# Performance work log

Measured on AMD Instinct MI355X. Metric: run time of the kernel, lower is better.

## Reference

```python
import jax, jax.numpy as jnp
import numpy as np

B, S, D = 1, 2048, 2048
H, HD = 16, 128  # n_heads, head_dim
ROPE_BASE = 100000.0


def setup_inputs() -> dict:
    key = jax.random.key(0)
    k0, k1, k2 = jax.random.split(key, 3)
    x = jax.random.normal(k0, (B, S, D), jnp.float32)
    # real RoPE table: (seq_len, head_dim//2, 2) holding (cos, sin)
    inv_freq = 1.0 / (ROPE_BASE ** (np.arange(0, HD, 2, dtype=np.float64) / HD))
    t = np.arange(S, dtype=np.float64)[:, None] * inv_freq[None, :]
    freqs_cis = jnp.asarray(np.stack([np.cos(t), np.sin(t)], axis=-1), jnp.float32)
    input_pos = jnp.arange(S, dtype=jnp.int32)
    Wqkv = jax.random.normal(k1, (D, 3 * D), jnp.float32) * (D ** -0.5)
    bqkv = jnp.zeros((3 * D,), jnp.float32)
    Wdense = jax.random.normal(k2, (D, D), jnp.float32) * (D ** -0.5)
    bdense = jnp.zeros((D,), jnp.float32)
    return {"x": x, "freqs_cis": freqs_cis, "input_pos": input_pos,
            "Wqkv": Wqkv, "bqkv": bqkv, "Wdense": Wdense, "bdense": bdense}


def apply_rotary_emb(x, freqs_cis):
    # x: [B, S, H, HD]; freqs_cis: [S, HD//2, 2]
    xs = x.reshape(*x.shape[:-1], -1, 2)  # [B,S,H,HD/2,2]
    fc = freqs_cis.reshape(1, xs.shape[1], 1, xs.shape[3], 2)
    out = jnp.stack([
        xs[..., 0] * fc[..., 0] - xs[..., 1] * fc[..., 1],
        xs[..., 1] * fc[..., 0] + xs[..., 0] * fc[..., 1],
    ], axis=-1)
    return out.reshape(x.shape).astype(x.dtype)


def reference(x, freqs_cis, input_pos, Wqkv, bqkv, Wdense, bdense):
    b, s, d = x.shape
    qkv = x @ Wqkv + bqkv                      # fused QKV projection
    q, k, v = jnp.split(qkv, 3, axis=-1)
    q = q.reshape(b, s, H, HD)
    k = k.reshape(b, s, H, HD)
    v = v.reshape(b, s, H, HD)
    q = apply_rotary_emb(q, freqs_cis)
    k = apply_rotary_emb(k, freqs_cis)
    # KV-cache update (cache batch = 1, max_seq = context_length)
    k_cache = jnp.zeros((1, S, H, HD), jnp.float32)
    v_cache = jnp.zeros((1, S, H, HD), jnp.float32)
    k_full = k_cache.at[:, input_pos].set(k)
    v_full = v_cache.at[:, input_pos].set(v)
    # causal SDPA in [B, H, S, HD] layout
    qh = q.transpose(0, 2, 1, 3)
    kh = k_full.transpose(0, 2, 1, 3)
    vh = v_full.transpose(0, 2, 1, 3)
    scale = HD ** -0.5
    scores = jnp.einsum('bhqd,bhkd->bhqk', qh, kh) * scale  # [B,H,S,S]
    causal = jnp.tril(jnp.ones((s, S), dtype=bool))
    scores = jnp.where(causal, scores, jnp.finfo(scores.dtype).min)
    attn = jax.nn.softmax(scores, axis=-1)
    ctx = jnp.einsum('bhqk,bhkd->bhqd', attn, vh)
    ctx = ctx.transpose(0, 2, 1, 3).reshape(b, s, d)
    return ctx @ Wdense + bdense
```

## Files before the change

### kernel.cpp

```cpp
#include <hip/hip_runtime.h>

#define S 2048
#define D 2048
#define H 16
#define HD 128
#define N3 6144

typedef __attribute__((ext_vector_type(8))) _Float16 f16x8;
typedef __attribute__((ext_vector_type(4))) float f32x4;
typedef unsigned short ushort_t;
typedef unsigned int uint_t;

__device__ __forceinline__ ushort_t f16_rne(float f) {
    _Float16 h = (_Float16)f;
    return __builtin_bit_cast(ushort_t, h);
}
__device__ __forceinline__ float f16_f32(ushort_t u) {
    return (float)__builtin_bit_cast(_Float16, u);
}

__global__ __launch_bounds__(256) void convert_f16_kernel(
    const float* __restrict__ in, ushort_t* __restrict__ hi)
{
    const int i = blockIdx.x * 256 + threadIdx.x;
    float4 v = ((const float4*)in)[i];
    ((ushort4*)hi)[i] = make_ushort4(f16_rne(v.x), f16_rne(v.y),
                                     f16_rne(v.z), f16_rne(v.w));
}

__global__ __launch_bounds__(256) void convert_t_kernel(
    const float* __restrict__ in, ushort_t* __restrict__ hi,
    int Kdim, int Ndim)
{
    __shared__ float tile[32][33];
    const int k0 = blockIdx.x * 32, n0 = blockIdx.y * 32;
    const int tx = threadIdx.x & 31, ty = threadIdx.x >> 5;
    #pragma unroll
    for (int r = 0; r < 4; r++)
        tile[ty + r * 8][tx] = in[(size_t)(k0 + ty + r * 8) * Ndim + n0 + tx];
    __syncthreads();
    const int n  = threadIdx.x >> 3;
    const int kc = (threadIdx.x & 7) * 4;
    const float v0 = tile[kc + 0][n], v1 = tile[kc + 1][n];
    const float v2 = tile[kc + 2][n], v3 = tile[kc + 3][n];
    const size_t off = (size_t)(n0 + n) * Kdim + k0 + kc;
    *(ushort4*)&hi[off] = make_ushort4(f16_rne(v0), f16_rne(v1),
                                       f16_rne(v2), f16_rne(v3));
}

__device__ __forceinline__ void gload16(const ushort_t* g, ushort_t* l) {
    __builtin_amdgcn_global_load_lds(
        (const __attribute__((address_space(1))) unsigned int*)g,
        (__attribute__((address_space(3))) unsigned int*)l, 16, 0, 0);
}

__device__ __forceinline__ void vwait8() { asm volatile("s_waitcnt vmcnt(8)" ::: "memory"); }
__device__ __forceinline__ void vwait4() { asm volatile("s_waitcnt vmcnt(4)" ::: "memory"); }
__device__ __forceinline__ void vwait0() { asm volatile("s_waitcnt vmcnt(0)" ::: "memory"); }
__device__ __forceinline__ void lwait0() { asm volatile("s_waitcnt lgkmcnt(0)" ::: "memory"); }

#define QNT 32

__device__ __forceinline__ void mm_core_8ph(
    const ushort_t* __restrict__ At, const ushort_t* __restrict__ Bt,
    ushort_t* lds, const int t, f32x4 (&acc)[4][4])
{
    const int w = t >> 6, lane = t & 63;
    const int lr = lane & 15, quad = lane >> 4;
    const int wm = (w & 1) * 64;
    const int wn = (w >> 1) * 64;

    const int srow = lane >> 2;
    const int scol = (lane & 3) * 8;
    const size_t goff0 = (size_t)(w * 16 + srow) * D + scol;
    const size_t goff1 = goff0 + (size_t)64 * D;
    const int ldst0 = w * 512;
    const int ldst1 = 2048 + w * 512;

    auto stage = [&](int j, int Tt) {
        const ushort_t* gb = (j & 1) ? Bt : At;
        const size_t off = (size_t)Tt * 64 + (j >> 1) * 32;
        ushort_t* dst = lds + (Tt & 1) * 16384 + j * 4096;
        gload16(gb + goff0 + off, dst + ldst0);
        gload16(gb + goff1 + off, dst + ldst1);
    };

    const int aro = (wm + lr) * 32 + quad * 8;
    const int bro = 4096 + (wn + lr) * 32 + quad * 8;

    stage(0, 0); stage(1, 0); stage(2, 0); stage(3, 0);
    stage(0, 1); stage(1, 1);
    vwait4();
    __builtin_amdgcn_sched_barrier(0);
    __builtin_amdgcn_s_barrier();

    f16x8 af[4], bf[4];

#define PH(kk, DOSTAGE, ST, WAITN)                                         \
    {                                                                      \
        const ushort_t* base = lds + (T & 1) * 16384 + (kk) * 8192;        \
        _Pragma("unroll")                                                  \
        for (int i = 0; i < 4; i++)                                        \
            af[i] = *(const f16x8*)&base[aro + i * 512];                   \
        _Pragma("unroll")                                                  \
        for (int n = 0; n < 4; n++)                                        \
            bf[n] = *(const f16x8*)&base[bro + n * 512];                   \
        if (DOSTAGE) {                                                     \
            stage((kk) ? 0 : 2, ST);                                       \
            stage((kk) ? 1 : 3, ST);                                       \
        }                                                                  \
        __builtin_amdgcn_s_barrier();                                      \
        lwait0();                                                          \
        __builtin_amdgcn_sched_barrier(0);                                 \
        __builtin_amdgcn_s_setprio(1);                                     \
        _Pragma("unroll")                                                  \
        for (int i = 0; i < 4; i++)                                        \
            _Pragma("unroll")                                              \
            for (int n = 0; n < 4; n++)                                    \
                acc[i][n] = __builtin_amdgcn_mfma_f32_16x16x32_f16(        \
                    af[i], bf[n], acc[i][n], 0, 0, 0);                     \
        __builtin_amdgcn_s_setprio(0);                                     \
        WAITN;                                                             \
        __builtin_amdgcn_s_barrier();                                      \
    }

    for (int T = 0; T < QNT - 2; T++) {
        PH(0, true, T + 1, vwait8());
        PH(1, true, T + 2, vwait8());
    }
    {
        const int T = QNT - 2;
        PH(0, true,  T + 1, vwait8());
        PH(1, false, 0,     vwait4());
    }
    {
        const int T = QNT - 1;
        PH(0, false, 0, vwait0());
        PH(1, false, 0, );
    }
#undef PH
}

__global__ __launch_bounds__(256, 2) void gemm_qkv_mfma(
    const ushort_t* __restrict__ xh,
    const ushort_t* __restrict__ Wth,
    const float* __restrict__ bias, const float* __restrict__ freqs,
    const int* __restrict__ input_pos,
    ushort_t* __restrict__ qhg, ushort_t* __restrict__ khg,
    ushort_t* __restrict__ vhg)
{
    __shared__ ushort_t lds[32768];
    const int t = threadIdx.x;
    const int col0 = blockIdx.x * 128;
    const int row0 = blockIdx.y * 128;

    f32x4 acc[4][4] = {};
    mm_core_8ph(xh + (size_t)row0 * D, Wth + (size_t)col0 * D, lds, t, acc);

    const int lane = t & 63;
    const int quad = lane >> 4;
    const int lr   = lane & 15;
    const int w = t >> 6;
    const int wm = (w & 1) * 64;
    const int wn = (w >> 1) * 64;

    const int which = col0 >> 11;
    const int hh = (col0 & 2047) >> 7;

    if (which == 2) {
        ushort_t* vh_b = vhg + (size_t)hh * HD * S;
        #pragma unroll
        for (int nt = 0; nt < 4; nt++) {
            const int d = wn + nt * 16 + lr;
            const float bsc = bias[col0 + d];
            #pragma unroll
            for (int mt = 0; mt < 4; mt++) {
                #pragma unroll
                for (int reg = 0; reg < 4; reg++) {
                    const int m = row0 + wm + mt * 16 + quad * 4 + reg;
                    const float v = acc[mt][nt][reg] + bsc;
                    vh_b[(size_t)d * S + input_pos[m]] = f16_rne(v);
                }
            }
        }
    } else {
        ushort_t* oh_b = ((which == 0) ? qhg : khg) + (size_t)hh * S * HD;
        #pragma unroll
        for (int nt = 0; nt < 4; nt++) {
            const int d = wn + nt * 16 + lr;
            const float bsc = bias[col0 + d];
            #pragma unroll
            for (int mt = 0; mt < 4; mt++) {
                #pragma unroll
                for (int reg = 0; reg < 4; reg++) {
                    const int m = row0 + wm + mt * 16 + quad * 4 + reg;
                    const float v = acc[mt][nt][reg] + bsc;
                    const float* fc = &freqs[((size_t)m * 64 + (d >> 1)) * 2];
                    const float cc = fc[0], ss = fc[1];
                    const float p = __shfl_xor(v, 1);
                    const float o = (d & 1) ? (v * cc + p * ss) : (v * cc - p * ss);
                    const ushort_t hv = f16_rne(o);
                    const int hp = __shfl_xor((int)hv, 1);
                    if (!(d & 1)) {
                        const int srowg = (which == 0) ? m : input_pos[m];
                        *(uint_t*)&oh_b[(size_t)srowg * HD + d] =
                            (uint_t)hv | ((uint_t)hp << 16);
                    }
                }
            }
        }
    }
}

__global__ __launch_bounds__(256, 2) void gemm_dense_mfma(
    const ushort_t* __restrict__ Ah,
    const ushort_t* __restrict__ Wth,
    const float* __restrict__ bias, float* __restrict__ out)
{
    __shared__ ushort_t lds[32768];
    const int t = threadIdx.x;
    const int col0 = blockIdx.x * 128;
    const int row0 = blockIdx.y * 128;

    f32x4 acc[4][4] = {};
    mm_core_8ph(Ah + (size_t)row0 * D, Wth + (size_t)col0 * D, lds, t, acc);

    const int lane = t & 63;
    const int quad = lane >> 4;
    const int lr   = lane & 15;
    const int w = t >> 6;
    const int wm = (w & 1) * 64;
    const int wn = (w >> 1) * 64;

    #pragma unroll
    for (int nt = 0; nt < 4; nt++) {
        const int n = col0 + wn + nt * 16 + lr;
        const float bsc = bias[n];
        #pragma unroll
        for (int mt = 0; mt < 4; mt++) {
            #pragma unroll
            for (int reg = 0; reg < 4; reg++) {
                const int m = row0 + wm + mt * 16 + quad * 4 + reg;
                const float o = acc[mt][nt][reg] + bsc;
                const float po = __shfl_xor(o, 1);
                if (!(n & 1))
                    *(float2*)&out[(size_t)m * D + n] = make_float2(o, po);
            }
        }
    }
}

__global__ __launch_bounds__(256, 2) void attn_mfma_kernel(
    const ushort_t* __restrict__ qhg, const ushort_t* __restrict__ khg,
    const ushort_t* __restrict__ vhg,
    float* __restrict__ Opart, float* __restrict__ MLpart)
{
    __shared__ ushort_t Khs[2][4096];
    __shared__ ushort_t Vhs[2][4096];
    __shared__ ushort_t Ps[64 * 32];

    const int bi   = blockIdx.x;
    const int h    = (bi & 7) + 8 * ((bi >> 3) & 1);
    const int half = (bi >> 4) & 1;
    const int qi   = bi >> 5;
    const int r = (h & 8) ? qi : (31 - qi);
    const int q0 = r * 64;
    const int nhalf = r + 1;
    const int kt0 = half * nhalf;
    const int kt1 = kt0 + nhalf;
    const int t = threadIdx.x;
    const int w = t >> 6, lane = t & 63;
    const int lr = lane & 15, quad = lane >> 4;

    const size_t qrow = (size_t)h * S + q0 + w * 16 + lr;
    f16x8 qf[4];
    #pragma unroll
    for (int ks = 0; ks < 4; ks++)
        qf[ks] = *(const f16x8*)&qhg[qrow * HD + ks * 32 + quad * 8];

    const ushort_t* kh_b = khg + (size_t)h * S * HD;
    const ushort_t* vh_b = vhg + (size_t)h * HD * S;

    const int keyq = lane >> 2;
    const int sub  = lane & 3;

    auto stage = [&](int kt, int buf) {
        const int k0 = kt * 32;
        #pragma unroll
        for (int hf = 0; hf < 2; hf++) {
            const size_t ksrc = (size_t)(k0 + hf * 16 + keyq) * HD + w * 32 + sub * 8;
            gload16(kh_b + ksrc, &Khs[buf][w * 1024 + hf * 512]);
            const int dim = w * 32 + hf * 16 + keyq;
            const size_t vsrc = (size_t)dim * S + k0 + sub * 8;
            gload16(vh_b + vsrc, &Vhs[buf][(w * 32 + hf * 16) * 32]);
        }
    };

    f32x4 O[8] = {};
    f32x4 Ol = {0.f, 0.f, 0.f, 0.f};
    float mrow[4];
    #pragma unroll
    for (int rr = 0; rr < 4; rr++) mrow[rr] = -1e30f;

    f16x8 onesv;
    #pragma unroll
    for (int i = 0; i < 8; i++) onesv[i] = (_Float16)1.0f;

    const float kSc = 0.08838834764831845f * 1.4426950408889634f;

    stage(kt0, 0);

    for (int kt = kt0; kt < kt1; kt++) {
        const int k0 = kt * 32;
        const int cur = (kt - kt0) & 1;
        __syncthreads();

        if (kt + 1 < kt1) stage(kt + 1, cur ^ 1);

        f32x4 sa[2];
        #pragma unroll
        for (int nt = 0; nt < 2; nt++) {
            f32x4 s = {0.f, 0.f, 0.f, 0.f};
            #pragma unroll
            for (int ks = 0; ks < 4; ks++) {
                f16x8 kf = *(const f16x8*)&Khs[cur][ks * 1024 + (nt * 16 + lr) * 32 + quad * 8];
                s = __builtin_amdgcn_mfma_f32_16x16x32_f16(qf[ks], kf, s, 0, 0, 0);
            }
            sa[nt] = s;
        }

        const int rowbase = q0 + w * 16 + quad * 4;
        const bool need_mask = (k0 + 31) > (q0 + w * 16);
        float alpha[4], pv0[4], pv1[4];
        #pragma unroll
        for (int rr = 0; rr < 4; rr++) {
            float z0 = sa[0][rr] * kSc;
            float z1 = sa[1][rr] * kSc;
            if (need_mask) {
                const int rowg = rowbase + rr;
                if (k0 + lr > rowg)      z0 = -1e30f;
                if (k0 + 16 + lr > rowg) z1 = -1e30f;
            }
            float rm = fmaxf(z0, z1);
            #pragma unroll
            for (int off = 1; off < 16; off <<= 1)
                rm = fmaxf(rm, __shfl_xor(rm, off));
            const float nm = fmaxf(mrow[rr], rm);
            alpha[rr] = exp2f(mrow[rr] - nm);
            pv0[rr] = exp2f(z0 - nm);
            pv1[rr] = exp2f(z1 - nm);
            mrow[rr] = nm;
        }

        #pragma unroll
        for (int rr = 0; rr < 4; rr++) {
            const int prow = (w * 16 + quad * 4 + rr) * 32;
            Ps[prow + lr]      = f16_rne(pv0[rr]);
            Ps[prow + 16 + lr] = f16_rne(pv1[rr]);
        }

        #pragma unroll
        for (int nt = 0; nt < 8; nt++)
            #pragma unroll
            for (int rr = 0; rr < 4; rr++)
                O[nt][rr] *= alpha[rr];
        #pragma unroll
        for (int rr = 0; rr < 4; rr++)
            Ol[rr] *= alpha[rr];
        const f16x8 pf = *(const f16x8*)&Ps[(w * 16 + lr) * 32 + quad * 8];
        #pragma unroll
        for (int nt = 0; nt < 8; nt++) {
            f16x8 vf = *(const f16x8*)&Vhs[cur][(nt * 16 + lr) * 32 + quad * 8];
            O[nt] = __builtin_amdgcn_mfma_f32_16x16x32_f16(pf, vf, O[nt], 0, 0, 0);
        }
        Ol = __builtin_amdgcn_mfma_f32_16x16x32_f16(pf, onesv, Ol, 0, 0, 0);
    }

    float* Ob = Opart + (size_t)bi * 64 * 128;
    #pragma unroll
    for (int rr = 0; rr < 4; rr++) {
        const int row = w * 16 + quad * 4 + rr;
        #pragma unroll
        for (int nt = 0; nt < 8; nt++)
            Ob[(size_t)row * 128 + nt * 16 + lr] = O[nt][rr];
        if (lr == 0) {
            MLpart[(size_t)bi * 128 + row * 2 + 0] = mrow[rr];
            MLpart[(size_t)bi * 128 + row * 2 + 1] = Ol[rr];
        }
    }
}

__global__ __launch_bounds__(128) void attn_combine_kernel(
    const float* __restrict__ Opart, const float* __restrict__ MLpart,
    ushort_t* __restrict__ ctxh)
{
    const int qt = blockIdx.x;
    const int h  = blockIdx.y;
    const int t  = threadIdx.x;
    const int b0 = h | (qt << 5);
    const int b1 = b0 | (1 << 4);
    const int r = (h & 8) ? qt : (31 - qt);
    const int q0 = r * 64;

    __shared__ float sc[64][2];
    if (t < 64) {
        const float m0 = MLpart[(size_t)b0 * 128 + t * 2 + 0];
        const float l0 = MLpart[(size_t)b0 * 128 + t * 2 + 1];
        const float m1 = MLpart[(size_t)b1 * 128 + t * 2 + 0];
        const float l1 = MLpart[(size_t)b1 * 128 + t * 2 + 1];
        const float m = fmaxf(m0, m1);
        const float a0 = exp2f(m0 - m), a1 = exp2f(m1 - m);
        const float inv = 1.0f / (l0 * a0 + l1 * a1);
        sc[t][0] = a0 * inv;
        sc[t][1] = a1 * inv;
    }
    __syncthreads();

    const float* O0 = Opart + (size_t)b0 * 64 * 128;
    const float* O1 = Opart + (size_t)b1 * 64 * 128;
    for (int row = 0; row < 64; row++) {
        const float o = O0[(size_t)row * 128 + t] * sc[row][0] +
                        O1[(size_t)row * 128 + t] * sc[row][1];
        ctxh[(size_t)(q0 + row) * D + h * HD + t] = f16_rne(o);
    }
}

__global__ __launch_bounds__(256) void gemm_qkv_kernel(
    const float* __restrict__ x, const float* __restrict__ W,
    const float* __restrict__ bias, const float* __restrict__ freqs,
    const int* __restrict__ input_pos,
    float* __restrict__ qb, float* __restrict__ kb, float* __restrict__ vb)
{
    __shared__ float As[16][68];
    __shared__ float Bs[16][64];
    const int bx = blockIdx.x;
    const int by = blockIdx.y;
    const int tid = threadIdx.x;
    const int tx = tid & 15, ty = tid >> 4;
    const int row0 = by * 64, col0 = bx * 64;
    const int am = tid >> 2;
    const int ak = (tid & 3) * 4;
    const int bk = tid >> 4;
    const int bn = (tid & 15) * 4;
    float acc[4][4] = {};
    for (int k0 = 0; k0 < D; k0 += 16) {
        float4 av = *(const float4*)&x[(size_t)(row0 + am) * D + k0 + ak];
        float4 bv = *(const float4*)&W[(size_t)(k0 + bk) * N3 + col0 + bn];
        __syncthreads();
        As[ak + 0][am] = av.x; As[ak + 1][am] = av.y;
        As[ak + 2][am] = av.z; As[ak + 3][am] = av.w;
        *(float4*)&Bs[bk][bn] = bv;
        __syncthreads();
        #pragma unroll
        for (int k = 0; k < 16; k++) {
            float4 a4 = *(const float4*)&As[k][ty * 4];
            float4 b4 = *(const float4*)&Bs[k][tx * 4];
            float a[4] = {a4.x, a4.y, a4.z, a4.w};
            float b[4] = {b4.x, b4.y, b4.z, b4.w};
            #pragma unroll
            for (int r = 0; r < 4; r++)
                #pragma unroll
                for (int c = 0; c < 4; c++)
                    acc[r][c] += a[r] * b[c];
        }
    }
    const int j0 = col0 + tx * 4;
    const int which = j0 >> 11;
    const int hh = (j0 & 2047) >> 7;
    const int d0 = j0 & 127;
    const float bv0 = bias[j0 + 0], bv1 = bias[j0 + 1];
    const float bv2 = bias[j0 + 2], bv3 = bias[j0 + 3];
    #pragma unroll
    for (int r = 0; r < 4; r++) {
        const int grow = row0 + ty * 4 + r;
        float v0 = acc[r][0] + bv0, v1 = acc[r][1] + bv1;
        float v2 = acc[r][2] + bv2, v3 = acc[r][3] + bv3;
        if (which == 2) {
            const int pos = input_pos[grow];
            float4 o4 = make_float4(v0, v1, v2, v3);
            *(float4*)&vb[((size_t)hh * S + pos) * HD + d0] = o4;
        } else {
            const float* fc = &freqs[((size_t)grow * 64 + (d0 >> 1)) * 2];
            float c0 = fc[0], s0 = fc[1], c1 = fc[2], s1 = fc[3];
            float o0 = v0 * c0 - v1 * s0, o1 = v1 * c0 + v0 * s0;
            float o2 = v2 * c1 - v3 * s1, o3 = v3 * c1 + v2 * s1;
            float4 o4 = make_float4(o0, o1, o2, o3);
            if (which == 0) {
                *(float4*)&qb[((size_t)hh * S + grow) * HD + d0] = o4;
            } else {
                const int pos = input_pos[grow];
                *(float4*)&kb[((size_t)hh * S + pos) * HD + d0] = o4;
            }
        }
    }
}

#define BQ 64
#define ABK 32
#define QSTR 132
#define KVSTR 132
#define PSTR 68

__global__ __launch_bounds__(256) void attn_kernel(
    const float* __restrict__ qb, const float* __restrict__ kb,
    const float* __restrict__ vb, float* __restrict__ ctx)
{
    __shared__ float Qs[BQ * QSTR];
    __shared__ float KV[ABK * KVSTR];
    __shared__ float Psf[ABK * PSTR];

    const int pa = blockIdx.x;
    const int h  = blockIdx.y;
    const int t  = threadIdx.x;
    const int ty = t >> 4, tx = t & 15;
    const int i0  = ty * 4;
    const int j0  = tx * 2;
    const int dd0 = tx * 8;
    const int lr = t >> 3;
    const int lc = (t & 7) * 4;

    const float* kbase = kb + (size_t)h * S * HD;
    const float* vbase = vb + (size_t)h * S * HD;
    const float kSc = 0.08838834764831845f * 1.4426950408889634f;

    for (int ph = 0; ph < 2; ph++) {
        const int r = (ph == 0) ? pa : 31 - pa;
        const int q0 = r * BQ;
        const int ntiles = 2 * r + 2;

        #pragma unroll
        for (int pp = 0; pp < 2; pp++) {
            const int iq = lr + pp * 32;
            const float* src = qb + ((size_t)h * S + q0 + iq) * HD;
            #pragma unroll
            for (int ch = 0; ch < 4; ch++)
                *(float4*)&Qs[iq * QSTR + lc + ch * 32] =
                    *(const float4*)&src[lc + ch * 32];
        }

        float O[4][8] = {};
        float m[4], l[4];
        #pragma unroll
        for (int rr = 0; rr < 4; rr++) { m[rr] = -1e30f; l[rr] = 0.f; }

        float4 kpref[4];
        #pragma unroll
        for (int ch = 0; ch < 4; ch++)
            kpref[ch] = *(const float4*)&kbase[(size_t)lr * HD + lc + ch * 32];

        __syncthreads();

        for (int kt = 0; kt < ntiles; kt++) {
            const int k0 = kt * ABK;

            #pragma unroll
            for (int ch = 0; ch < 4; ch++)
                *(float4*)&KV[lr * KVSTR + lc + ch * 32] = kpref[ch];
            __syncthreads();

            float4 vpref[4];
            #pragma unroll
            for (int ch = 0; ch < 4; ch++)
                vpref[ch] = *(const float4*)&vbase[(size_t)(k0 + lr) * HD + lc + ch * 32];

            float acc[4][2] = {};
            #pragma unroll 4
            for (int d0 = 0; d0 < HD; d0 += 4) {
                float4 ka = *(const float4*)&KV[(j0 + 0) * KVSTR + d0];
                float4 kb4 = *(const float4*)&KV[(j0 + 1) * KVSTR + d0];
                #pragma unroll
                for (int rr = 0; rr < 4; rr++) {
                    float4 q4 = *(const float4*)&Qs[(i0 + rr) * QSTR + d0];
                    acc[rr][0] += q4.x * ka.x + q4.y * ka.y + q4.z * ka.z + q4.w * ka.w;
                    acc[rr][1] += q4.x * kb4.x + q4.y * kb4.y + q4.z * kb4.z + q4.w * kb4.w;
                }
            }

            const bool need_mask = (k0 + ABK - 1) > q0;
            float p[4][2], alpha[4];
            #pragma unroll
            for (int rr = 0; rr < 4; rr++) {
                float z0 = acc[rr][0] * kSc;
                float z1 = acc[rr][1] * kSc;
                if (need_mask) {
                    if (k0 + j0 + 0 > q0 + i0 + rr) z0 = -1e30f;
                    if (k0 + j0 + 1 > q0 + i0 + rr) z1 = -1e30f;
                }
                float rmax = fmaxf(z0, z1);
                #pragma unroll
                for (int off = 1; off < 16; off <<= 1)
                    rmax = fmaxf(rmax, __shfl_xor(rmax, off, 16));
                const float nm = fmaxf(m[rr], rmax);
                alpha[rr] = exp2f(m[rr] - nm);
                p[rr][0] = exp2f(z0 - nm);
                p[rr][1] = exp2f(z1 - nm);
                float ts = p[rr][0] + p[rr][1];
                #pragma unroll
                for (int off = 1; off < 16; off <<= 1)
                    ts += __shfl_xor(ts, off, 16);
                l[rr] = l[rr] * alpha[rr] + ts;
                m[rr] = nm;
            }
            __syncthreads();

            #pragma unroll
            for (int ch = 0; ch < 4; ch++)
                *(float4*)&KV[lr * KVSTR + lc + ch * 32] = vpref[ch];
            *(float4*)&Psf[(j0 + 0) * PSTR + i0] =
                make_float4(p[0][0], p[1][0], p[2][0], p[3][0]);
            *(float4*)&Psf[(j0 + 1) * PSTR + i0] =
                make_float4(p[0][1], p[1][1], p[2][1], p[3][1]);
            if (kt + 1 < ntiles) {
                #pragma unroll
                for (int ch = 0; ch < 4; ch++)
                    kpref[ch] = *(const float4*)&kbase[(size_t)(k0 + ABK + lr) * HD + lc + ch * 32];
            }
            __syncthreads();

            #pragma unroll
            for (int rr = 0; rr < 4; rr++)
                #pragma unroll
                for (int c = 0; c < 8; c++)
                    O[rr][c] *= alpha[rr];
            #pragma unroll 4
            for (int j = 0; j < ABK; j++) {
                float4 pj = *(const float4*)&Psf[j * PSTR + i0];
                float4 v0 = *(const float4*)&KV[j * KVSTR + dd0];
                float4 v1 = *(const float4*)&KV[j * KVSTR + dd0 + 4];
                const float pr[4] = {pj.x, pj.y, pj.z, pj.w};
                const float vv[8] = {v0.x, v0.y, v0.z, v0.w, v1.x, v1.y, v1.z, v1.w};
                #pragma unroll
                for (int rr = 0; rr < 4; rr++)
                    #pragma unroll
                    for (int c = 0; c < 8; c++)
                        O[rr][c] += pr[rr] * vv[c];
            }
            __syncthreads();
        }

        #pragma unroll
        for (int rr = 0; rr < 4; rr++) {
            const float inv = 1.0f / l[rr];
            const int qg = q0 + i0 + rr;
            float4 o0 = make_float4(O[rr][0] * inv, O[rr][1] * inv,
                                    O[rr][2] * inv, O[rr][3] * inv);
            float4 o1 = make_float4(O[rr][4] * inv, O[rr][5] * inv,
                                    O[rr][6] * inv, O[rr][7] * inv);
            float* dst = &ctx[((size_t)qg * H + h) * HD + dd0];
            *(float4*)&dst[0] = o0;
            *(float4*)&dst[4] = o1;
        }
        __syncthreads();
    }
}

__global__ __launch_bounds__(256) void gemm_dense_kernel(
    const float* __restrict__ A, const float* __restrict__ W,
    const float* __restrict__ bias, float* __restrict__ out)
{
    __shared__ float As[16][68];
    __shared__ float Bs[16][64];
    const int bx = blockIdx.x;
    const int by = blockIdx.y;
    const int tid = threadIdx.x;
    const int tx = tid & 15, ty = tid >> 4;
    const int row0 = by * 64, col0 = bx * 64;
    const int am = tid >> 2;
    const int ak = (tid & 3) * 4;
    const int bk = tid >> 4;
    const int bn = (tid & 15) * 4;
    float acc[4][4] = {};
    for (int k0 = 0; k0 < D; k0 += 16) {
        float4 av = *(const float4*)&A[(size_t)(row0 + am) * D + k0 + ak];
        float4 bv = *(const float4*)&W[(size_t)(k0 + bk) * D + col0 + bn];
        __syncthreads();
        As[ak + 0][am] = av.x; As[ak + 1][am] = av.y;
        As[ak + 2][am] = av.z; As[ak + 3][am] = av.w;
        *(float4*)&Bs[bk][bn] = bv;
        __syncthreads();
        #pragma unroll
        for (int k = 0; k < 16; k++) {
            float4 a4 = *(const float4*)&As[k][ty * 4];
            float4 b4 = *(const float4*)&Bs[k][tx * 4];
            float a[4] = {a4.x, a4.y, a4.z, a4.w};
            float b[4] = {b4.x, b4.y, b4.z, b4.w};
            #pragma unroll
            for (int r = 0; r < 4; r++)
                #pragma unroll
                for (int c = 0; c < 4; c++)
                    acc[r][c] += a[r] * b[c];
        }
    }
    const int j0 = col0 + tx * 4;
    const float bv0 = bias[j0 + 0], bv1 = bias[j0 + 1];
    const float bv2 = bias[j0 + 2], bv3 = bias[j0 + 3];
    #pragma unroll
    for (int r = 0; r < 4; r++) {
        const int grow = row0 + ty * 4 + r;
        float4 o4 = make_float4(acc[r][0] + bv0, acc[r][1] + bv1,
                                acc[r][2] + bv2, acc[r][3] + bv3);
        *(float4*)&out[(size_t)grow * D + j0] = o4;
    }
}

extern "C" void kernel_launch(void* const* d_in, const int* in_sizes, int n_in,
                              void* d_out, int out_size, void* d_ws, size_t ws_size,
                              hipStream_t stream) {
    const float* x      = (const float*)d_in[0];
    const float* freqs  = (const float*)d_in[1];
    const int*   pos    = (const int*)d_in[2];
    const float* Wqkv   = (const float*)d_in[3];
    const float* bqkv   = (const float*)d_in[4];
    const float* Wdense = (const float*)d_in[5];
    const float* bdense = (const float*)d_in[6];
    float* out = (float*)d_out;

    const size_t nSD = (size_t)S * D;
    const size_t nW1 = (size_t)D * N3;
    const size_t nOP = (size_t)1024 * 64 * 128;
    const size_t nML = (size_t)1024 * 128;

    const size_t needed =
        (6 * nSD + nW1) * sizeof(ushort_t) + (nOP + nML) * sizeof(float);

    if (ws_size >= needed) {
        ushort_t* qh   = (ushort_t*)d_ws;
        ushort_t* kh   = qh + nSD;
        ushort_t* vh   = kh + nSD;
        ushort_t* ctxh = vh + nSD;
        ushort_t* xh   = ctxh + nSD;
        ushort_t* Wth  = xh + nSD;
        ushort_t* Wdth = Wth + nW1;
        float* Opart = (float*)(Wdth + nSD);
        float* MLpart = Opart + nOP;

        convert_f16_kernel<<<nSD / 4 / 256, 256, 0, stream>>>(x, xh);
        dim3 gt1(D / 32, N3 / 32);
        convert_t_kernel<<<gt1, 256, 0, stream>>>(Wqkv, Wth, D, N3);
        dim3 gt2(D / 32, D / 32);
        convert_t_kernel<<<gt2, 256, 0, stream>>>(Wdense, Wdth, D, D);

        dim3 g1(N3 / 128, S / 128);
        gemm_qkv_mfma<<<g1, 256, 0, stream>>>(xh, Wth, bqkv, freqs,
                                              pos, qh, kh, vh);
        attn_mfma_kernel<<<1024, 256, 0, stream>>>(qh, kh, vh,
                                                   Opart, MLpart);
        dim3 gc(32, H);
        attn_combine_kernel<<<gc, 128, 0, stream>>>(Opart, MLpart, ctxh);
        dim3 g3(D / 128, S / 128);
        gemm_dense_mfma<<<g3, 256, 0, stream>>>(ctxh, Wdth, bdense, out);
    } else {
        float* qb  = (float*)d_ws;
        float* kb  = qb + (size_t)H * S * HD;
        float* vb  = kb + (size_t)H * S * HD;
        float* ctx = vb + (size_t)H * S * HD;
        dim3 g1(N3 / 64, S / 64);
        gemm_qkv_kernel<<<g1, 256, 0, stream>>>(x, Wqkv, bqkv, freqs, pos, qb, kb, vb);
        dim3 g2(16, H);
        attn_kernel<<<g2, 256, 0, stream>>>(qb, kb, vb, ctx);
        dim3 g3(D / 64, S / 64);
        gemm_dense_kernel<<<g3, 256, 0, stream>>>(ctx, Wdense, bdense, out);
    }
}
```

Measured before the change: 340.7 us.

## Restructure GEMM core with swizzled LDS, block remap, and larger attention key tiles

Replaces the 8-phase GEMM mainloop with a simpler per-K-tile loop that loads both 32-wide halves of a 64-wide K tile into XOR-swizzled LDS, to cut bank conflicts and barriers. Remaps GEMM block indices in groups of 8 to improve L2 reuse. Doubles the attention key tile from 32 to 64 with a swizzled V layout, and rebalances the causal split across the two halves. These trade fewer barriers and better locality for more registers and LDS per block, which can lower occupancy.

```diff
diff --git a/kernel.cpp b/kernel.cpp
--- a/kernel.cpp
+++ b/kernel.cpp
@@ -55,13 +55,12 @@
 }
 
 __device__ __forceinline__ void vwait8() { asm volatile("s_waitcnt vmcnt(8)" ::: "memory"); }
-__device__ __forceinline__ void vwait4() { asm volatile("s_waitcnt vmcnt(4)" ::: "memory"); }
 __device__ __forceinline__ void vwait0() { asm volatile("s_waitcnt vmcnt(0)" ::: "memory"); }
 __device__ __forceinline__ void lwait0() { asm volatile("s_waitcnt lgkmcnt(0)" ::: "memory"); }
 
 #define QNT 32
 
-__device__ __forceinline__ void mm_core_8ph(
+__device__ __forceinline__ void mm_core_v3(
     const ushort_t* __restrict__ At, const ushort_t* __restrict__ Bt,
     ushort_t* lds, const int t, f32x4 (&acc)[4][4])
 {
@@ -70,75 +69,68 @@
     const int wm = (w & 1) * 64;
     const int wn = (w >> 1) * 64;
 
-    const int srow = lane >> 2;
-    const int scol = (lane & 3) * 8;
-    const size_t goff0 = (size_t)(w * 16 + srow) * D + scol;
-    const size_t goff1 = goff0 + (size_t)64 * D;
-    const int ldst0 = w * 512;
-    const int ldst1 = 2048 + w * 512;
-
-    auto stage = [&](int j, int Tt) {
-        const ushort_t* gb = (j & 1) ? Bt : At;
-        const size_t off = (size_t)Tt * 64 + (j >> 1) * 32;
-        ushort_t* dst = lds + (Tt & 1) * 16384 + j * 4096;
-        gload16(gb + goff0 + off, dst + ldst0);
-        gload16(gb + goff1 + off, dst + ldst1);
+    const int trow = t >> 3;
+    const int tcol = ((t & 7) ^ ((t >> 3) & 7)) * 8;
+    const int ldsw = w * 512;
+
+    auto stageAB = [&](int Tt) {
+        ushort_t* dbase = lds + (Tt & 1) * 16384;
+        const size_t koff = (size_t)Tt * 64 + tcol;
+        #pragma unroll
+        for (int i = 0; i < 4; i++) {
+            gload16(At + (size_t)(i * 32 + trow) * D + koff,
+                    dbase + i * 2048 + ldsw);
+            gload16(Bt + (size_t)(i * 32 + trow) * D + koff,
+                    dbase + 8192 + i * 2048 + ldsw);
+        }
     };
 
-    const int aro = (wm + lr) * 32 + quad * 8;
-    const int bro = 4096 + (wn + lr) * 32 + quad * 8;
-
-    stage(0, 0); stage(1, 0); stage(2, 0); stage(3, 0);
-    stage(0, 1); stage(1, 1);
-    vwait4();
+    const int aoff = (wm + lr) * 64;
+    const int boff = 8192 + (wn + lr) * 64;
+    const int sw0 = ((0 * 4 + quad) ^ (lr & 7)) * 8;
+    const int sw1 = ((1 * 4 + quad) ^ (lr & 7)) * 8;
+
+    stageAB(0);
+    stageAB(1);
+    vwait8();
     __builtin_amdgcn_sched_barrier(0);
     __builtin_amdgcn_s_barrier();
 
-    f16x8 af[4], bf[4];
-
-#define PH(kk, DOSTAGE, ST, WAITN)                                         \
-    {                                                                      \
-        const ushort_t* base = lds + (T & 1) * 16384 + (kk) * 8192;        \
-        _Pragma("unroll")                                                  \
-        for (int i = 0; i < 4; i++)                                        \
-            af[i] = *(const f16x8*)&base[aro + i * 512];                   \
-        _Pragma("unroll")                                                  \
-        for (int n = 0; n < 4; n++)                                        \
-            bf[n] = *(const f16x8*)&base[bro + n * 512];                   \
-        if (DOSTAGE) {                                                     \
-            stage((kk) ? 0 : 2, ST);                                       \
-            stage((kk) ? 1 : 3, ST);                                       \
-        }                                                                  \
-        __builtin_amdgcn_s_barrier();                                      \
-        lwait0();                                                          \
-        __builtin_amdgcn_sched_barrier(0);                                 \
-        __builtin_amdgcn_s_setprio(1);                                     \
-        _Pragma("unroll")                                                  \
-        for (int i = 0; i < 4; i++)                                        \
-            _Pragma("unroll")                                              \
-            for (int n = 0; n < 4; n++)                                    \
-                acc[i][n] = __builtin_amdgcn_mfma_f32_16x16x32_f16(        \
-                    af[i], bf[n], acc[i][n], 0, 0, 0);                     \
-        __builtin_amdgcn_s_setprio(0);                                     \
-        WAITN;                                                             \
-        __builtin_amdgcn_s_barrier();                                      \
-    }
-
-    for (int T = 0; T < QNT - 2; T++) {
-        PH(0, true, T + 1, vwait8());
-        PH(1, true, T + 2, vwait8());
-    }
-    {
-        const int T = QNT - 2;
-        PH(0, true,  T + 1, vwait8());
-        PH(1, false, 0,     vwait4());
-    }
-    {
-        const int T = QNT - 1;
-        PH(0, false, 0, vwait0());
-        PH(1, false, 0, );
-    }
-#undef PH
+    for (int T = 0; T < QNT; T++) {
+        const ushort_t* base = lds + (T & 1) * 16384;
+        f16x8 a0[4], a1[4], b0[4], b1[4];
+        #pragma unroll
+        for (int i = 0; i < 4; i++) {
+            a0[i] = *(const f16x8*)&base[aoff + i * 1024 + sw0];
+            a1[i] = *(const f16x8*)&base[aoff + i * 1024 + sw1];
+            b0[i] = *(const f16x8*)&base[boff + i * 1024 + sw0];
+            b1[i] = *(const f16x8*)&base[boff + i * 1024 + sw1];
+        }
+        lwait0();
+        __builtin_amdgcn_sched_barrier(0);
+        __builtin_amdgcn_s_barrier();
+
+        if (T < QNT - 2) stageAB(T + 2);
+
+        __builtin_amdgcn_s_setprio(1);
+        #pragma unroll
+        for (int i = 0; i < 4; i++)
+            #pragma unroll
+            for (int n = 0; n < 4; n++)
+                acc[i][n] = __builtin_amdgcn_mfma_f32_16x16x32_f16(
+                    a0[i], b0[n], acc[i][n], 0, 0, 0);
+        #pragma unroll
+        for (int i = 0; i < 4; i++)
+            #pragma unroll
+            for (int n = 0; n < 4; n++)
+                acc[i][n] = __builtin_amdgcn_mfma_f32_16x16x32_f16(
+                    a1[i], b1[n], acc[i][n], 0, 0, 0);
+        __builtin_amdgcn_s_setprio(0);
+
+        if (T < QNT - 2)      vwait8();
+        else if (T == QNT - 2) vwait0();
+        __builtin_amdgcn_s_barrier();
+    }
 }
 
 __global__ __launch_bounds__(256, 2) void gemm_qkv_mfma(
@@ -151,11 +143,13 @@
 {
     __shared__ ushort_t lds[32768];
     const int t = threadIdx.x;
-    const int col0 = blockIdx.x * 128;
-    const int row0 = blockIdx.y * 128;
+    const int bid = blockIdx.y * 48 + blockIdx.x;
+    const int swz = (bid & 7) * 96 + (bid >> 3);
+    const int col0 = (swz % 48) * 128;
+    const int row0 = (swz / 48) * 128;
 
     f32x4 acc[4][4] = {};
-    mm_core_8ph(xh + (size_t)row0 * D, Wth + (size_t)col0 * D, lds, t, acc);
+    mm_core_v3(xh + (size_t)row0 * D, Wth + (size_t)col0 * D, lds, t, acc);
 
     const int lane = t & 63;
     const int quad = lane >> 4;
@@ -219,11 +213,13 @@
 {
     __shared__ ushort_t lds[32768];
     const int t = threadIdx.x;
-    const int col0 = blockIdx.x * 128;
-    const int row0 = blockIdx.y * 128;
+    const int bid = blockIdx.y * 16 + blockIdx.x;
+    const int swz = (bid & 7) * 32 + (bid >> 3);
+    const int col0 = (swz & 15) * 128;
+    const int row0 = (swz >> 4) * 128;
 
     f32x4 acc[4][4] = {};
-    mm_core_8ph(Ah + (size_t)row0 * D, Wth + (size_t)col0 * D, lds, t, acc);
+    mm_core_v3(Ah + (size_t)row0 * D, Wth + (size_t)col0 * D, lds, t, acc);
 
     const int lane = t & 63;
     const int quad = lane >> 4;
@@ -255,9 +251,9 @@
     const ushort_t* __restrict__ vhg,
     float* __restrict__ Opart, float* __restrict__ MLpart)
 {
-    __shared__ ushort_t Khs[2][4096];
-    __shared__ ushort_t Vhs[2][4096];
-    __shared__ ushort_t Ps[64 * 32];
+    __shared__ ushort_t Khs[2][8192];
+    __shared__ ushort_t Vhs[2][8192];
+    __shared__ ushort_t Ps[4096];
 
     const int bi   = blockIdx.x;
     const int h    = (bi & 7) + 8 * ((bi >> 3) & 1);
@@ -265,9 +261,10 @@
     const int qi   = bi >> 5;
     const int r = (h & 8) ? qi : (31 - qi);
     const int q0 = r * 64;
-    const int nhalf = r + 1;
-    const int kt0 = half * nhalf;
-    const int kt1 = kt0 + nhalf;
+    const int T = r + 1;
+    const int n0 = (T + 1) >> 1;
+    const int ktbeg = half ? n0 : 0;
+    const int ktend = half ? T : n0;
     const int t = threadIdx.x;
     const int w = t >> 6, lane = t & 63;
     const int lr = lane & 15, quad = lane >> 4;
@@ -282,17 +279,19 @@
     const ushort_t* vh_b = vhg + (size_t)h * HD * S;
 
     const int keyq = lane >> 2;
-    const int sub  = lane & 3;
+    const int ksub = (lane & 3) * 8;
+    const int vrow8 = lane >> 3;
+    const int vsub = ((lane & 7) ^ (lane >> 3)) * 8;
 
     auto stage = [&](int kt, int buf) {
-        const int k0 = kt * 32;
-        #pragma unroll
-        for (int hf = 0; hf < 2; hf++) {
-            const size_t ksrc = (size_t)(k0 + hf * 16 + keyq) * HD + w * 32 + sub * 8;
-            gload16(kh_b + ksrc, &Khs[buf][w * 1024 + hf * 512]);
-            const int dim = w * 32 + hf * 16 + keyq;
-            const size_t vsrc = (size_t)dim * S + k0 + sub * 8;
-            gload16(vh_b + vsrc, &Vhs[buf][(w * 32 + hf * 16) * 32]);
+        const int k0 = kt * 64;
+        #pragma unroll
+        for (int hf = 0; hf < 4; hf++) {
+            const size_t ksrc = (size_t)(k0 + hf * 16 + keyq) * HD + w * 32 + ksub;
+            gload16(kh_b + ksrc, &Khs[buf][w * 2048 + hf * 512]);
+            const int dim = w * 32 + hf * 8 + vrow8;
+            const size_t vsrc = (size_t)dim * S + k0 + vsub;
+            gload16(vh_b + vsrc, &Vhs[buf][(w * 32 + hf * 8) * 64]);
         }
     };
 
@@ -308,55 +307,63 @@
 
     const float kSc = 0.08838834764831845f * 1.4426950408889634f;
 
-    stage(kt0, 0);
-
-    for (int kt = kt0; kt < kt1; kt++) {
-        const int k0 = kt * 32;
-        const int cur = (kt - kt0) & 1;
+    if (ktbeg < ktend) stage(ktbeg, 0);
+
+    for (int kt = ktbeg; kt < ktend; kt++) {
+        const int k0 = kt * 64;
+        const int cur = (kt - ktbeg) & 1;
         __syncthreads();
 
-        if (kt + 1 < kt1) stage(kt + 1, cur ^ 1);
-
-        f32x4 sa[2];
-        #pragma unroll
-        for (int nt = 0; nt < 2; nt++) {
+        if (kt + 1 < ktend) stage(kt + 1, cur ^ 1);
+
+        f32x4 sa[4];
+        #pragma unroll
+        for (int nt = 0; nt < 4; nt++) {
             f32x4 s = {0.f, 0.f, 0.f, 0.f};
             #pragma unroll
             for (int ks = 0; ks < 4; ks++) {
-                f16x8 kf = *(const f16x8*)&Khs[cur][ks * 1024 + (nt * 16 + lr) * 32 + quad * 8];
+                f16x8 kf = *(const f16x8*)&Khs[cur][ks * 2048 + (nt * 16 + lr) * 32 + quad * 8];
                 s = __builtin_amdgcn_mfma_f32_16x16x32_f16(qf[ks], kf, s, 0, 0, 0);
             }
             sa[nt] = s;
         }
 
         const int rowbase = q0 + w * 16 + quad * 4;
-        const bool need_mask = (k0 + 31) > (q0 + w * 16);
-        float alpha[4], pv0[4], pv1[4];
+        const bool need_mask = (k0 + 63) > (q0 + w * 16);
+        float alpha[4], pv[4][4];
         #pragma unroll
         for (int rr = 0; rr < 4; rr++) {
             float z0 = sa[0][rr] * kSc;
             float z1 = sa[1][rr] * kSc;
+            float z2 = sa[2][rr] * kSc;
+            float z3 = sa[3][rr] * kSc;
             if (need_mask) {
                 const int rowg = rowbase + rr;
                 if (k0 + lr > rowg)      z0 = -1e30f;
                 if (k0 + 16 + lr > rowg) z1 = -1e30f;
-            }
-            float rm = fmaxf(z0, z1);
+                if (k0 + 32 + lr > rowg) z2 = -1e30f;
+                if (k0 + 48 + lr > rowg) z3 = -1e30f;
+            }
+            float rm = fmaxf(fmaxf(z0, z1), fmaxf(z2, z3));
             #pragma unroll
             for (int off = 1; off < 16; off <<= 1)
                 rm = fmaxf(rm, __shfl_xor(rm, off));
             const float nm = fmaxf(mrow[rr], rm);
             alpha[rr] = exp2f(mrow[rr] - nm);
-            pv0[rr] = exp2f(z0 - nm);
-            pv1[rr] = exp2f(z1 - nm);
+            pv[0][rr] = exp2f(z0 - nm);
+            pv[1][rr] = exp2f(z1 - nm);
+            pv[2][rr] = exp2f(z2 - nm);
+            pv[3][rr] = exp2f(z3 - nm);
             mrow[rr] = nm;
         }
 
         #pragma unroll
         for (int rr = 0; rr < 4; rr++) {
             const int prow = (w * 16 + quad * 4 + rr) * 32;
-            Ps[prow + lr]      = f16_rne(pv0[rr]);
-            Ps[prow + 16 + lr] = f16_rne(pv1[rr]);
+            #pragma unroll
+            for (int nt = 0; nt < 4; nt++)
+                Ps[(nt >> 1) * 2048 + prow + (nt & 1) * 16 + lr] =
+                    f16_rne(pv[nt][rr]);
         }
 
         #pragma unroll
@@ -367,13 +374,18 @@
         #pragma unroll
         for (int rr = 0; rr < 4; rr++)
             Ol[rr] *= alpha[rr];
-        const f16x8 pf = *(const f16x8*)&Ps[(w * 16 + lr) * 32 + quad * 8];
-        #pragma unroll
-        for (int nt = 0; nt < 8; nt++) {
-            f16x8 vf = *(const f16x8*)&Vhs[cur][(nt * 16 + lr) * 32 + quad * 8];
-            O[nt] = __builtin_amdgcn_mfma_f32_16x16x32_f16(pf, vf, O[nt], 0, 0, 0);
-        }
-        Ol = __builtin_amdgcn_mfma_f32_16x16x32_f16(pf, onesv, Ol, 0, 0, 0);
+
+        #pragma unroll
+        for (int kc = 0; kc < 2; kc++) {
+            const f16x8 pf = *(const f16x8*)&Ps[kc * 2048 + (w * 16 + lr) * 32 + quad * 8];
+            #pragma unroll
+            for (int nt = 0; nt < 8; nt++) {
+                f16x8 vf = *(const f16x8*)&Vhs[cur][(nt * 16 + lr) * 64 +
+                                                    (((kc * 4 + quad) ^ (lr & 7)) * 8)];
+                O[nt] = __builtin_amdgcn_mfma_f32_16x16x32_f16(pf, vf, O[nt], 0, 0, 0);
+            }
+            Ol = __builtin_amdgcn_mfma_f32_16x16x32_f16(pf, onesv, Ol, 0, 0, 0);
+        }
     }
 
     float* Ob = Opart + (size_t)bi * 64 * 128;
```

Measured after the change: 361.2 us. +6.0%, slower.
